# Kernel tuning notes

Measured on AMD Instinct MI355X. Metric: run time of the kernel, lower is better.

## Reference

```python
import jax, jax.numpy as jnp
import numpy as np

WINDOW = 11
SIGMA = 1.5
CHANNELS = 3
C1 = 0.01 ** 2
C2 = 0.03 ** 2


def _gaussian_kernel(size=WINDOW, sigma=SIGMA, channels=CHANNELS):
    coords = jnp.arange(size, dtype=jnp.float32) - size // 2
    g = jnp.exp(-coords ** 2 / (2.0 * sigma ** 2))
    g = jnp.outer(g, g)
    g = g / g.sum()
    # depthwise kernel: [C, 1, K, K] (OIHW with feature_group_count=C)
    return jnp.broadcast_to(g[None, None], (channels, 1, size, size))


def _dwconv(x, kernel):
    # x: [N, C, H, W]; SAME padding, depthwise (groups = C)
    pad = WINDOW // 2
    return jax.lax.conv_general_dilated(
        x, kernel,
        window_strides=(1, 1),
        padding=[(pad, pad), (pad, pad)],
        dimension_numbers=('NCHW', 'OIHW', 'NCHW'),
        feature_group_count=CHANNELS,
    )


def setup_inputs() -> dict:
    key = jax.random.key(0)
    k1, k2 = jax.random.split(key)
    shape = (16, 3, 512, 512)
    pred = jax.random.uniform(k1, shape, dtype=jnp.float32)
    target = jax.random.uniform(k2, shape, dtype=jnp.float32)
    return {"pred": pred, "target": target}


def reference(pred, target):
    kernel = _gaussian_kernel().astype(pred.dtype)
    mu_p = _dwconv(pred, kernel)
    mu_t = _dwconv(target, kernel)
    mu_p2 = mu_p * mu_p
    mu_t2 = mu_t * mu_t
    mu_pt = mu_p * mu_t
    sigma_p2 = _dwconv(pred * pred, kernel) - mu_p2
    sigma_t2 = _dwconv(target * target, kernel) - mu_t2
    sigma_pt = _dwconv(pred * target, kernel) - mu_pt
    ssim_map = ((2.0 * mu_pt + C1) * (2.0 * sigma_pt + C2)) / (
        (mu_p2 + mu_t2 + C1) * (sigma_p2 + sigma_t2 + C2)
    )
    return 1.0 - ssim_map.mean()
```

## Files before the change

kernel.cpp:

```cpp
#include <hip/hip_runtime.h>
#include <math.h>

#define IMG_H 512
#define IMG_W 512
#define NSLOT 64
#define SAB_S 56
#define HT_S  56

typedef _Float16 f16x4 __attribute__((ext_vector_type(4)));
typedef _Float16 f16x8 __attribute__((ext_vector_type(8)));
typedef float    f32x4 __attribute__((ext_vector_type(4)));

__device__ __forceinline__ f16x8 build_frag(int which, int l)
{
    const int lln = l & 15, llg = l >> 4;
    f16x8 f;
    #pragma unroll
    for (int j = 0; j < 8; ++j) {
        int idx = llg * 8 + j - lln - (which ? 0 : 3);
        float d = (float)(idx - 5);
        float v = 0.26601173f * exp2f(-d * d * 0.32059889f);
        f[j] = (_Float16)(((unsigned)idx <= 10u) ? v : 0.0f);
    }
    return f;
}

__global__ __launch_bounds__(256, 6)
void ssim_main(const float* __restrict__ pred, const float* __restrict__ targ,
               float* __restrict__ partial, double* __restrict__ acc, int mode)
{
    __shared__ _Float16 sAB[2][48][SAB_S];
    __shared__ _Float16 hT[4][32][HT_S];

    const int tid  = threadIdx.x;
    const int lane = tid & 63, wave = tid >> 6;
    const int ln   = lane & 15, lg = lane >> 4;

    const int tx = blockIdx.x, ty = blockIdx.y, img = blockIdx.z;
    const float* __restrict__ p = pred + (size_t)img * (IMG_H * IMG_W);
    const float* __restrict__ t = targ + (size_t)img * (IMG_H * IMG_W);
    const int gr0 = ty * 32 - 5;
    const int wo  = tx * 32 - 8;

    const f16x8 Bw  = build_frag(0, lane);
    const f16x8 A2w = build_frag(1, lane);
    const f32x4 z = {0.f, 0.f, 0.f, 0.f};

    for (int i = tid; i < 48 * 6; i += 256) {
        const int r = i / 6, g = i - 6 * r;
        const int gr = gr0 + r;
        const bool in = (gr >= 0) && (gr < IMG_H) &&
                        !(tx == 0 && g == 0) && !(tx == 15 && g == 5);
        float4 p0 = {0,0,0,0}, p1 = {0,0,0,0}, t0 = {0,0,0,0}, t1 = {0,0,0,0};
        if (in) {
            const float* bp = p + (size_t)gr * IMG_W + (wo + 8 * g);
            const float* bt = t + (size_t)gr * IMG_W + (wo + 8 * g);
            p0 = ((const float4*)bp)[0]; p1 = ((const float4*)bp)[1];
            t0 = ((const float4*)bt)[0]; t1 = ((const float4*)bt)[1];
        }
        *(f16x8*)&sAB[0][r][8 * g] = f16x8{
            (_Float16)(p0.x + t0.x), (_Float16)(p0.y + t0.y),
            (_Float16)(p0.z + t0.z), (_Float16)(p0.w + t0.w),
            (_Float16)(p1.x + t1.x), (_Float16)(p1.y + t1.y),
            (_Float16)(p1.z + t1.z), (_Float16)(p1.w + t1.w)};
        *(f16x8*)&sAB[1][r][8 * g] = f16x8{
            (_Float16)(p0.x - t0.x), (_Float16)(p0.y - t0.y),
            (_Float16)(p0.z - t0.z), (_Float16)(p0.w - t0.w),
            (_Float16)(p1.x - t1.x), (_Float16)(p1.y - t1.y),
            (_Float16)(p1.z - t1.z), (_Float16)(p1.w - t1.w)};
    }
    __syncthreads();

    auto do_tile = [&](int tt) {
        const int rt = tt >> 1, ct = tt & 1;
        const int rowbase = rt * 16;
        f16x8 s8 = *(const f16x8*)&sAB[0][rowbase + ln][ct * 16 + lg * 8];
        f16x8 d8 = *(const f16x8*)&sAB[1][rowbase + ln][ct * 16 + lg * 8];
        f16x8 fq[4];
        fq[0] = s8; fq[1] = d8;
        fq[2] = s8 * s8; fq[3] = d8 * d8;
        const int ocol = ct * 16 + ln;
        const int orow = rowbase + lg * 4;
        #pragma unroll
        for (int q = 0; q < 4; ++q) {
            f32x4 dd = __builtin_amdgcn_mfma_f32_16x16x32_f16(fq[q], Bw, z, 0, 0, 0);
            *(f16x4*)&hT[q][ocol][orow] =
                f16x4{(_Float16)dd[0], (_Float16)dd[1], (_Float16)dd[2], (_Float16)dd[3]};
        }
    };
    do_tile(wave);
    if (wave < 2) do_tile(wave + 4);
    __syncthreads();

    float lsum = 0.f;
    {
        const int ctv = wave & 1, rtv = wave >> 1;
        const int ocol  = ctv * 16 + ln;
        const int rbase = rtv * 16 + lg * 8;
        f32x4 accq[4];
        #pragma unroll
        for (int q = 0; q < 4; ++q) {
            f16x8 b = *(const f16x8*)&hT[q][ocol][rbase];
            accq[q] = __builtin_amdgcn_mfma_f32_16x16x32_f16(A2w, b, z, 0, 0, 0);
        }
        const float C1 = 1e-4f, C2 = 9e-4f;
        #pragma unroll
        for (int r = 0; r < 4; ++r) {
            float F1 = accq[0][r], F2 = accq[1][r];
            float F3 = accq[2][r], F4 = accq[3][r];
            float a = F1 * F1, b = F2 * F2;
            float mpmt2 = 0.5f * (a - b);
            float msq   = 0.5f * (a + b);
            float cpt2  = 0.5f * (F3 - F4) - mpmt2;
            float vsum  = 0.5f * (F3 + F4) - msq;
            float num = (mpmt2 + C1) * (cpt2 + C2);
            float den = (msq + C1) * (vsum + C2);
            lsum = fmaf(num, __builtin_amdgcn_rcpf(den), lsum);
        }
    }

    #pragma unroll
    for (int off = 32; off > 0; off >>= 1)
        lsum += __shfl_down(lsum, off, 64);
    if (lane == 0) {
        const int bid = (blockIdx.z * gridDim.y + blockIdx.y) * gridDim.x + blockIdx.x;
        if (mode == 0) partial[bid * 4 + wave] = lsum;
        else atomicAdd(&acc[(bid * 4 + wave) & (NSLOT - 1)], (double)lsum);
    }
}

__global__ void ssim_init(double* acc)
{
    if (threadIdx.x < NSLOT) acc[threadIdx.x] = 0.0;
}

__global__ __launch_bounds__(1024)
void ssim_fin_slots(const float* __restrict__ partial, float* __restrict__ out,
                    int n4, double inv_n)
{
    __shared__ double red[16];
    double s = 0.0;
    const int tid = threadIdx.x;
    for (int i = tid; i < n4; i += 1024) {
        float4 v = ((const float4*)partial)[i];
        s += (double)v.x + (double)v.y + (double)v.z + (double)v.w;
    }
    #pragma unroll
    for (int off = 32; off > 0; off >>= 1)
        s += __shfl_down(s, off, 64);
    if ((tid & 63) == 0) red[tid >> 6] = s;
    __syncthreads();
    if (tid == 0) {
        double tot = 0.0;
        #pragma unroll
        for (int w = 0; w < 16; ++w) tot += red[w];
        out[0] = (float)(1.0 - tot * inv_n);
    }
}

__global__ void ssim_fin_atomic(const double* __restrict__ acc, float* __restrict__ out,
                                double inv_n)
{
    if (threadIdx.x == 0) {
        double s = 0.0;
        for (int i = 0; i < NSLOT; ++i) s += acc[i];
        out[0] = (float)(1.0 - s * inv_n);
    }
}

extern "C" void kernel_launch(void* const* d_in, const int* in_sizes, int n_in,
                              void* d_out, int out_size, void* d_ws, size_t ws_size,
                              hipStream_t stream)
{
    const float* pred = (const float*)d_in[0];
    const float* targ = (const float*)d_in[1];
    float* out = (float*)d_out;

    const long long total = (long long)in_sizes[0];
    const int n_img = (int)(total / (IMG_H * IMG_W));
    dim3 grid(IMG_W / 32, IMG_H / 32, n_img);
    const int nblk = grid.x * grid.y * grid.z;
    const int nslots = nblk * 4;
    const double inv_n = 1.0 / (double)total;

    if (ws_size >= (size_t)nslots * sizeof(float)) {
        float* partial = (float*)d_ws;
        hipLaunchKernelGGL(ssim_main, grid, dim3(256), 0, stream,
                           pred, targ, partial, (double*)nullptr, 0);
        hipLaunchKernelGGL(ssim_fin_slots, dim3(1), dim3(1024), 0, stream,
                           partial, out, nslots / 4, inv_n);
    } else {
        double* acc = (double*)d_ws;
        hipLaunchKernelGGL(ssim_init, dim3(1), dim3(64), 0, stream, acc);
        hipLaunchKernelGGL(ssim_main, grid, dim3(256), 0, stream,
                           pred, targ, (float*)nullptr, acc, 1);
        hipLaunchKernelGGL(ssim_fin_atomic, dim3(1), dim3(1), 0, stream,
                           acc, out, inv_n);
    }
}
```

Measured before the change: 140.5 us.

## Load tiles directly into MFMA fragments, remap blocks for XCD locality, table-based weights

Removes the shared-memory staging buffer and its barrier: each wave now loads its input fragment from global memory straight into registers before the horizontal MFMA pass. Block indices are remapped so consecutive blocks on each of the 8 XCDs process adjacent tiles, aiming for better L2 reuse of the overlapping halos. The Gaussian fragments now come from a constant table instead of per-lane exp2 computation, and the occupancy hint rises from 6 to 8 blocks. The cost is redundant global loads of overlapping halo rows across waves, and the table lookups are dynamically indexed.

```diff
diff --git a/kernel.cpp b/kernel.cpp
--- a/kernel.cpp
+++ b/kernel.cpp
@@ -4,78 +4,84 @@
 #define IMG_H 512
 #define IMG_W 512
 #define NSLOT 64
-#define SAB_S 56
 #define HT_S  56
 
 typedef _Float16 f16x4 __attribute__((ext_vector_type(4)));
 typedef _Float16 f16x8 __attribute__((ext_vector_type(8)));
 typedef float    f32x4 __attribute__((ext_vector_type(4)));
 
-__device__ __forceinline__ f16x8 build_frag(int which, int l)
-{
-    const int lln = l & 15, llg = l >> 4;
+__device__ const _Float16 WPAD[52] = {
+    (_Float16)0.f,(_Float16)0.f,(_Float16)0.f,(_Float16)0.f,(_Float16)0.f,(_Float16)0.f,
+    (_Float16)0.f,(_Float16)0.f,(_Float16)0.f,(_Float16)0.f,(_Float16)0.f,(_Float16)0.f,
+    (_Float16)0.f,(_Float16)0.f,(_Float16)0.f,(_Float16)0.f,(_Float16)0.f,(_Float16)0.f,
+    (_Float16)0.00102838f, (_Float16)0.00759876f, (_Float16)0.03600077f,
+    (_Float16)0.10936065f, (_Float16)0.21300554f, (_Float16)0.26601173f,
+    (_Float16)0.21300554f, (_Float16)0.10936065f, (_Float16)0.03600077f,
+    (_Float16)0.00759876f, (_Float16)0.00102838f,
+    (_Float16)0.f,(_Float16)0.f,(_Float16)0.f,(_Float16)0.f,(_Float16)0.f,(_Float16)0.f,
+    (_Float16)0.f,(_Float16)0.f,(_Float16)0.f,(_Float16)0.f,(_Float16)0.f,(_Float16)0.f,
+    (_Float16)0.f,(_Float16)0.f,(_Float16)0.f,(_Float16)0.f,(_Float16)0.f,(_Float16)0.f,
+    (_Float16)0.f,(_Float16)0.f,(_Float16)0.f,(_Float16)0.f,(_Float16)0.f
+};
+
+__device__ __forceinline__ f16x8 frag_from_tab(int base)
+{
     f16x8 f;
     #pragma unroll
-    for (int j = 0; j < 8; ++j) {
-        int idx = llg * 8 + j - lln - (which ? 0 : 3);
-        float d = (float)(idx - 5);
-        float v = 0.26601173f * exp2f(-d * d * 0.32059889f);
-        f[j] = (_Float16)(((unsigned)idx <= 10u) ? v : 0.0f);
-    }
+    for (int j = 0; j < 8; ++j) f[j] = WPAD[base + j];
     return f;
 }
 
-__global__ __launch_bounds__(256, 6)
+__global__ __launch_bounds__(256, 8)
 void ssim_main(const float* __restrict__ pred, const float* __restrict__ targ,
                float* __restrict__ partial, double* __restrict__ acc, int mode)
 {
-    __shared__ _Float16 sAB[2][48][SAB_S];
     __shared__ _Float16 hT[4][32][HT_S];
 
     const int tid  = threadIdx.x;
     const int lane = tid & 63, wave = tid >> 6;
     const int ln   = lane & 15, lg = lane >> 4;
 
-    const int tx = blockIdx.x, ty = blockIdx.y, img = blockIdx.z;
+    const int bid   = ((blockIdx.z << 4) + blockIdx.y) * 16 + blockIdx.x;
+    const int chunk = (int)gridDim.z << 5;
+    const int nb    = (bid & 7) * chunk + (bid >> 3);
+    const int img   = nb >> 8;
+    const int rem   = nb & 255;
+    const int ty    = rem >> 4, tx = rem & 15;
+
     const float* __restrict__ p = pred + (size_t)img * (IMG_H * IMG_W);
     const float* __restrict__ t = targ + (size_t)img * (IMG_H * IMG_W);
     const int gr0 = ty * 32 - 5;
     const int wo  = tx * 32 - 8;
 
-    const f16x8 Bw  = build_frag(0, lane);
-    const f16x8 A2w = build_frag(1, lane);
+    const f16x8 Bw = frag_from_tab(15 + lg * 8 - ln);
     const f32x4 z = {0.f, 0.f, 0.f, 0.f};
 
-    for (int i = tid; i < 48 * 6; i += 256) {
-        const int r = i / 6, g = i - 6 * r;
-        const int gr = gr0 + r;
+    auto do_tile = [&](int tt) {
+        const int rt = tt >> 1, ct = tt & 1;
+        const int rowbase = rt * 16;
+        const int gr = gr0 + rowbase + ln;
+        const int gc = wo + ct * 16 + lg * 8;
         const bool in = (gr >= 0) && (gr < IMG_H) &&
-                        !(tx == 0 && g == 0) && !(tx == 15 && g == 5);
+                        !(tx == 0 && ct == 0 && lg == 0) &&
+                        !(tx == 15 && ct == 1 && lg == 3);
         float4 p0 = {0,0,0,0}, p1 = {0,0,0,0}, t0 = {0,0,0,0}, t1 = {0,0,0,0};
         if (in) {
-            const float* bp = p + (size_t)gr * IMG_W + (wo + 8 * g);
-            const float* bt = t + (size_t)gr * IMG_W + (wo + 8 * g);
+            const float* bp = p + (size_t)gr * IMG_W + gc;
+            const float* bt = t + (size_t)gr * IMG_W + gc;
             p0 = ((const float4*)bp)[0]; p1 = ((const float4*)bp)[1];
             t0 = ((const float4*)bt)[0]; t1 = ((const float4*)bt)[1];
         }
-        *(f16x8*)&sAB[0][r][8 * g] = f16x8{
+        f16x8 s8 = f16x8{
             (_Float16)(p0.x + t0.x), (_Float16)(p0.y + t0.y),
             (_Float16)(p0.z + t0.z), (_Float16)(p0.w + t0.w),
             (_Float16)(p1.x + t1.x), (_Float16)(p1.y + t1.y),
             (_Float16)(p1.z + t1.z), (_Float16)(p1.w + t1.w)};
-        *(f16x8*)&sAB[1][r][8 * g] = f16x8{
+        f16x8 d8 = f16x8{
             (_Float16)(p0.x - t0.x), (_Float16)(p0.y - t0.y),
             (_Float16)(p0.z - t0.z), (_Float16)(p0.w - t0.w),
             (_Float16)(p1.x - t1.x), (_Float16)(p1.y - t1.y),
             (_Float16)(p1.z - t1.z), (_Float16)(p1.w - t1.w)};
-    }
-    __syncthreads();
-
-    auto do_tile = [&](int tt) {
-        const int rt = tt >> 1, ct = tt & 1;
-        const int rowbase = rt * 16;
-        f16x8 s8 = *(const f16x8*)&sAB[0][rowbase + ln][ct * 16 + lg * 8];
-        f16x8 d8 = *(const f16x8*)&sAB[1][rowbase + ln][ct * 16 + lg * 8];
         f16x8 fq[4];
         fq[0] = s8; fq[1] = d8;
         fq[2] = s8 * s8; fq[3] = d8 * d8;
@@ -90,6 +96,8 @@
     };
     do_tile(wave);
     if (wave < 2) do_tile(wave + 4);
+
+    const f16x8 A2w = frag_from_tab(18 + lg * 8 - ln);
     __syncthreads();
 
     float lsum = 0.f;
@@ -123,9 +131,8 @@
     for (int off = 32; off > 0; off >>= 1)
         lsum += __shfl_down(lsum, off, 64);
     if (lane == 0) {
-        const int bid = (blockIdx.z * gridDim.y + blockIdx.y) * gridDim.x + blockIdx.x;
-        if (mode == 0) partial[bid * 4 + wave] = lsum;
-        else atomicAdd(&acc[(bid * 4 + wave) & (NSLOT - 1)], (double)lsum);
+        if (mode == 0) partial[nb * 4 + wave] = lsum;
+        else atomicAdd(&acc[(nb * 4 + wave) & (NSLOT - 1)], (double)lsum);
     }
 }
 
```

Measured after the change: 150.2 us. 1.07x slower.
